# Kernel tuning notes

Hardware: AMD Instinct MI355X
Metric: run time of the kernel (lower is better)

The kernel has to match this reference:

```python
import jax, jax.numpy as jnp
import numpy as np

IN_F = 4096
OUT_F = 4096
N_VALS = 4096
N_TOKENS = 4096


def setup_inputs() -> dict:
    key = jax.random.key(0)
    k_x, k_v, k_i = jax.random.split(key, 3)
    x = jax.random.normal(k_x, (N_TOKENS, IN_F), dtype=jnp.float32)
    # codebook of memristor conductance differences (sorted, as in load_values)
    values = jnp.sort(jax.random.normal(k_v, (N_VALS,), dtype=jnp.float32))
    w_idx = jax.random.randint(k_i, (OUT_F, IN_F), 0, N_VALS, dtype=jnp.int64)
    bias = jnp.zeros((OUT_F,), dtype=jnp.float32)
    return {"x": x, "values": values, "w_idx": w_idx, "bias": bias}


def reference(x, values, w_idx, bias):
    # dequantize weight from codebook: (out_f, in_f)
    weight = values[w_idx]
    # F.linear(x, weight, bias) == x @ weight.T + bias
    return jnp.einsum("ti,oi->to", x, weight) + bias
```

## Files before the change

kernel.cpp:

```cpp
#include <hip/hip_runtime.h>
#include <hip/hip_bf16.h>
#include <stdint.h>

typedef unsigned short u16;
typedef __bf16 bf16x8 __attribute__((ext_vector_type(8)));
typedef float  f32x4  __attribute__((ext_vector_type(4)));
typedef u16    u16x8  __attribute__((ext_vector_type(8)));
typedef u16    u16x4  __attribute__((ext_vector_type(4)));

__device__ __forceinline__ u16 f2bf(float f) {
  union { float f; unsigned u; } v; v.f = f;
  unsigned u = v.u;
  unsigned r = u + 0x7FFFu + ((u >> 16) & 1u);
  return (u16)(r >> 16);
}

__device__ __forceinline__ void gld_lds16(const void* g, void* l) {
  __builtin_amdgcn_global_load_lds(
      (const __attribute__((address_space(1))) void*)g,
      (__attribute__((address_space(3))) void*)l, 16, 0, 0);
}

__global__ void detect_idx_width(const unsigned* __restrict__ w, int* __restrict__ flag) {
  unsigned v = w[threadIdx.x * 2 + 1];
  unsigned long long any = __ballot(v != 0u);
  if (threadIdx.x == 0) *flag = (any != 0ull) ? 1 : 0;
}

__global__ __launch_bounds__(256) void cvt_x_kernel(const float4* __restrict__ x,
                                                    u16* __restrict__ xb, long n8) {
  long i = (long)blockIdx.x * blockDim.x + threadIdx.x;
  long stride = (long)gridDim.x * blockDim.x;
  for (; i < n8; i += stride) {
    float4 a = x[2 * i];
    float4 b = x[2 * i + 1];
    u16x8 r;
    r[0] = f2bf(a.x); r[1] = f2bf(a.y); r[2] = f2bf(a.z); r[3] = f2bf(a.w);
    r[4] = f2bf(b.x); r[5] = f2bf(b.y); r[6] = f2bf(b.z); r[7] = f2bf(b.w);
    *(u16x8*)(xb + 8 * i) = r;
  }
}

__global__ __launch_bounds__(256) void dequant_w_kernel(const int4* __restrict__ widx,
                                                        const float* __restrict__ values,
                                                        u16* __restrict__ wb,
                                                        const int* __restrict__ flag, long n4) {
  const bool is32 = (*flag != 0);
  long i = (long)blockIdx.x * blockDim.x + threadIdx.x;
  long stride = (long)gridDim.x * blockDim.x;
  for (; i < n4; i += stride) {
    int i0, i1, i2, i3;
    if (is32) {
      int4 v = widx[i];
      i0 = v.x; i1 = v.y; i2 = v.z; i3 = v.w;
    } else {
      int4 a = widx[2 * i];
      int4 b = widx[2 * i + 1];
      i0 = a.x; i1 = a.z; i2 = b.x; i3 = b.z;
    }
    u16x4 r;
    r[0] = f2bf(values[i0]); r[1] = f2bf(values[i1]);
    r[2] = f2bf(values[i2]); r[3] = f2bf(values[i3]);
    *(u16x4*)(wb + 4 * i) = r;
  }
}

#define VMW(n) asm volatile("s_waitcnt vmcnt(" #n ")" ::: "memory")
#define LGKM0  asm volatile("s_waitcnt lgkmcnt(0)" ::: "memory")
#define SB0    __builtin_amdgcn_sched_barrier(0)
#define PH_BAR __builtin_amdgcn_s_barrier()

__global__ __launch_bounds__(512, 2) void gemm256_kernel(
    const u16* __restrict__ Xb, const u16* __restrict__ Wb,
    const float* __restrict__ bias, float* __restrict__ C,
    int Nout, int Kin) {
  __shared__ __align__(16) char lds[163840];

  const int tid  = threadIdx.x;
  const int lane = tid & 63;
  const int wave = tid >> 6;
  const int wr = wave >> 2;
  const int wc = wave & 3;

  const int nwg = gridDim.x;
  const int bid = blockIdx.x;
  const int q8 = nwg >> 3, r8 = nwg & 7;
  const int xcd = bid & 7;
  const int wg = (xcd < r8 ? xcd * (q8 + 1) : r8 * (q8 + 1) + (xcd - r8) * q8) + (bid >> 3);

  const int tiles_n = Nout / 256;
  const long brow = (long)(wg / tiles_n) * 256;
  const long bcol = (long)(wg % tiles_n) * 256;

  const size_t rowbytes = (size_t)Kin * 2;

  const int f0  = tid * 16;
  const int f1  = f0 + 8192;
  const int rS0 = f0 >> 7;
  const int rS1 = rS0 + 64;
  const int cS  = (f0 & 127) ^ ((rS0 & 7) << 4);

  const char* gA00 = (const char*)Xb + (size_t)(brow +       rS0) * rowbytes + cS;
  const char* gA01 = (const char*)Xb + (size_t)(brow +       rS1) * rowbytes + cS;
  const char* gA10 = (const char*)Xb + (size_t)(brow + 128 + rS0) * rowbytes + cS;
  const char* gA11 = (const char*)Xb + (size_t)(brow + 128 + rS1) * rowbytes + cS;
  const char* gB00 = (const char*)Wb + (size_t)(bcol +       rS0) * rowbytes + cS;
  const char* gB01 = (const char*)Wb + (size_t)(bcol +       rS1) * rowbytes + cS;
  const char* gB10 = (const char*)Wb + (size_t)(bcol + 128 + rS0) * rowbytes + cS;
  const char* gB11 = (const char*)Wb + (size_t)(bcol + 128 + rS1) * rowbytes + cS;

#define STAGE_AH(base_, h, t) { \
  gld_lds16(gA##h##0 + (size_t)(t) * 128, lds + (base_) + (h) * 16384 + f0); \
  gld_lds16(gA##h##1 + (size_t)(t) * 128, lds + (base_) + (h) * 16384 + f1); }
#define STAGE_BH(base_, h, t) { \
  gld_lds16(gB##h##0 + (size_t)(t) * 128, lds + (base_) + (h) * 16384 + f0); \
  gld_lds16(gB##h##1 + (size_t)(t) * 128, lds + (base_) + (h) * 16384 + f1); }

  const int fr   = lane & 15;
  const int kb   = (lane >> 4) * 16;
  const int xsw  = (fr & 7) << 4;
  const int colx0 = kb ^ xsw;
  const int colx1 = (64 + kb) ^ xsw;
  const int aOff = wr * 16384 + fr * 128;
  const int bOff = (wc >> 1) * 16384 + ((wc & 1) * 64 + fr) * 128;

  bf16x8 afr[2][2];
  bf16x8 bfrE[4][2];
  bf16x8 bfrO[4][2];
  f32x4  acc[8][4] = {};

#define READ_AQ(abase_, q) { \
  const char* ab = lds + (abase_) + aOff + (q) * 4096; \
  afr[0][0] = *(const bf16x8*)(ab + colx0); \
  afr[0][1] = *(const bf16x8*)(ab + colx1); \
  afr[1][0] = *(const bf16x8*)(ab + 2048 + colx0); \
  afr[1][1] = *(const bf16x8*)(ab + 2048 + colx1); }

#define READ_BPF(bbase_, dst, lo) { \
  const char* bb = lds + (bbase_) + bOff; \
  dst[(lo)][0]     = *(const bf16x8*)(bb + (lo) * 2048 + colx0); \
  dst[(lo)][1]     = *(const bf16x8*)(bb + (lo) * 2048 + colx1); \
  dst[(lo) + 1][0] = *(const bf16x8*)(bb + ((lo) + 1) * 2048 + colx0); \
  dst[(lo) + 1][1] = *(const bf16x8*)(bb + ((lo) + 1) * 2048 + colx1); }

#define MFMA_Q(q, B) { \
  __builtin_amdgcn_s_setprio(1); \
  _Pragma("unroll") for (int m2 = 0; m2 < 2; ++m2) \
  _Pragma("unroll") for (int ni = 0; ni < 4; ++ni) { \
    acc[(q)*2+m2][ni] = __builtin_amdgcn_mfma_f32_16x16x32_bf16(afr[m2][0], B[ni][0], acc[(q)*2+m2][ni], 0, 0, 0); \
    acc[(q)*2+m2][ni] = __builtin_amdgcn_mfma_f32_16x16x32_bf16(afr[m2][1], B[ni][1], acc[(q)*2+m2][ni], 0, 0, 0); } \
  __builtin_amdgcn_s_setprio(0); }

#define PHASE2(AB, q, B, EXTRA, WT) { \
  READ_AQ(AB, q); \
  EXTRA; \
  SB0; PH_BAR; LGKM0; SB0; \
  MFMA_Q(q, B); \
  SB0; WT; PH_BAR; }

  const int aB0 = 0, aB1 = 32768;
  int bR0 = 65536, bR1 = 98304, bR2 = 131072;
  const int NT = Kin >> 6;

  STAGE_AH(aB0, 0, 0); STAGE_AH(aB0, 1, 0);
  STAGE_BH(bR0, 0, 0); STAGE_BH(bR0, 1, 0);
  if (NT > 1) { STAGE_BH(bR1, 0, 1); STAGE_BH(bR1, 1, 1); }
  if (NT > 2) { STAGE_BH(bR2, 0, 2); STAGE_BH(bR2, 1, 2); }
  VMW(0);
  PH_BAR;
  READ_BPF(bR0, bfrE, 0); READ_BPF(bR0, bfrE, 2);

  const int NITER = NT >> 1;
  for (int i = 0; i < NITER; ++i) {
    const int t0 = i * 2;
    const bool gA2 = (t0 + 2 < NT);
    const bool gB3 = (t0 + 3 < NT);
    const bool gB4 = (t0 + 4 < NT);

    PHASE2(aB0, 0, bfrE, STAGE_AH(aB1, 0, t0 + 1), (void)0);
    PHASE2(aB0, 1, bfrE, { READ_BPF(bR1, bfrO, 0); STAGE_AH(aB1, 1, t0 + 1); }, (void)0);
    PHASE2(aB0, 2, bfrE, { READ_BPF(bR1, bfrO, 2); if (gB3) STAGE_BH(bR0, 0, t0 + 3); }, (void)0);
    PHASE2(aB0, 3, bfrE, { if (gB3) STAGE_BH(bR0, 1, t0 + 3); },
           { if (gB3) { VMW(2); } else { VMW(0); } });

    PHASE2(aB1, 0, bfrO, { if (gA2) STAGE_AH(aB0, 0, t0 + 2); }, (void)0);
    PHASE2(aB1, 1, bfrO, { if (gA2) { READ_BPF(bR2, bfrE, 0); STAGE_AH(aB0, 1, t0 + 2); } }, (void)0);
    PHASE2(aB1, 2, bfrO, { if (gA2) READ_BPF(bR2, bfrE, 2); if (gB4) STAGE_BH(bR1, 0, t0 + 4); }, (void)0);
    PHASE2(aB1, 3, bfrO, { if (gB4) STAGE_BH(bR1, 1, t0 + 4); },
           { if (gB4) { VMW(2); } else { VMW(0); } });

    int tmp = bR0; bR0 = bR2; bR2 = bR1; bR1 = tmp;
  }

  const int cm = (lane >> 4) * 4;
  const int cn = lane & 15;
  float bv[4];
#pragma unroll
  for (int ni = 0; ni < 4; ++ni) bv[ni] = bias[bcol + wc * 64 + ni * 16 + cn];

#pragma unroll
  for (int mi = 0; mi < 8; ++mi) {
    const long row0 = brow + wr * 128 + mi * 16 + cm;
#pragma unroll
    for (int ni = 0; ni < 4; ++ni) {
      const long col = bcol + wc * 64 + ni * 16 + cn;
#pragma unroll
      for (int j = 0; j < 4; ++j)
        C[(row0 + j) * (long)Nout + col] = acc[mi][ni][j] + bv[ni];
    }
  }
#undef STAGE_AH
#undef STAGE_BH
#undef READ_AQ
#undef READ_BPF
#undef MFMA_Q
#undef PHASE2
}

__global__ __launch_bounds__(256, 2) void gemm128_kernel(
    const u16* __restrict__ Xb, const u16* __restrict__ Wb,
    const float* __restrict__ bias, float* __restrict__ C,
    int Nout, int Kin) {
  __shared__ __align__(16) u16 As[128 * 32];
  __shared__ __align__(16) u16 Bs[128 * 32];
  const int tid  = threadIdx.x;
  const int lane = tid & 63;
  const int wave = tid >> 6;
  const int wr = wave >> 1, wc = wave & 1;
  const int nwg = gridDim.x, bid = blockIdx.x;
  const int q = nwg >> 3, r8 = nwg & 7;
  const int xcd = bid & 7;
  const int wg = (xcd < r8 ? xcd * (q + 1) : r8 * (q + 1) + (xcd - r8) * q) + (bid >> 3);
  const int tiles_n = Nout / 128;
  const long brow = (long)(wg / tiles_n) * 128;
  const long bcol = (long)(wg % tiles_n) * 128;
  const int f0 = tid * 16, f1 = f0 + 4096;
  const size_t rowbytes = (size_t)Kin * 2;
  const char* gA0 = (const char*)Xb + (size_t)(brow + (f0 >> 6)) * rowbytes + (f0 & 63);
  const char* gA1 = (const char*)Xb + (size_t)(brow + (f1 >> 6)) * rowbytes + (f1 & 63);
  const char* gB0 = (const char*)Wb + (size_t)(bcol + (f0 >> 6)) * rowbytes + (f0 & 63);
  const char* gB1 = (const char*)Wb + (size_t)(bcol + (f1 >> 6)) * rowbytes + (f1 & 63);
  char* lA0 = (char*)As + f0; char* lA1 = (char*)As + f1;
  char* lB0 = (char*)Bs + f0; char* lB1 = (char*)Bs + f1;
  const int fr = lane & 15, kb = (lane >> 4) * 16;
  const char* aptr[4]; const char* bptr[4];
#pragma unroll
  for (int i = 0; i < 4; ++i) {
    aptr[i] = (const char*)As + (wr * 64 + i * 16 + fr) * 64 + kb;
    bptr[i] = (const char*)Bs + (wc * 64 + i * 16 + fr) * 64 + kb;
  }
  f32x4 acc[4][4] = {};
  for (int kk = 0; kk < Kin; kk += 32) {
    const size_t ko = (size_t)kk * 2;
    gld_lds16(gA0 + ko, lA0); gld_lds16(gA1 + ko, lA1);
    gld_lds16(gB0 + ko, lB0); gld_lds16(gB1 + ko, lB1);
    __syncthreads();
    bf16x8 a[4], b[4];
#pragma unroll
    for (int i = 0; i < 4; ++i) a[i] = *(const bf16x8*)aptr[i];
#pragma unroll
    for (int i = 0; i < 4; ++i) b[i] = *(const bf16x8*)bptr[i];
#pragma unroll
    for (int mi = 0; mi < 4; ++mi)
#pragma unroll
      for (int ni = 0; ni < 4; ++ni)
        acc[mi][ni] = __builtin_amdgcn_mfma_f32_16x16x32_bf16(a[mi], b[ni], acc[mi][ni], 0, 0, 0);
    __syncthreads();
  }
  const int cm = (lane >> 4) * 4, cn = lane & 15;
  float bv[4];
#pragma unroll
  for (int ni = 0; ni < 4; ++ni) bv[ni] = bias[bcol + wc * 64 + ni * 16 + cn];
#pragma unroll
  for (int mi = 0; mi < 4; ++mi) {
    const long row0 = brow + wr * 64 + mi * 16 + cm;
#pragma unroll
    for (int ni = 0; ni < 4; ++ni) {
      const long col = bcol + wc * 64 + ni * 16 + cn;
#pragma unroll
      for (int j = 0; j < 4; ++j)
        C[(row0 + j) * (long)Nout + col] = acc[mi][ni][j] + bv[ni];
    }
  }
}

__global__ void fallback_kernel(const float* __restrict__ x, const float* __restrict__ values,
                                const int* __restrict__ widx, const float* __restrict__ bias,
                                float* __restrict__ out, const int* __restrict__ flag,
                                int NT, int IF, int OF) {
  const int o = blockIdx.x * blockDim.x + threadIdx.x;
  const int t = blockIdx.y;
  if (o >= OF || t >= NT) return;
  const bool is32 = (*flag != 0);
  const float* xr = x + (size_t)t * IF;
  float sum = 0.f;
  if (is32) {
    const int* w = widx + (size_t)o * IF;
    for (int k = 0; k < IF; ++k) sum += xr[k] * values[w[k]];
  } else {
    const long long* w = (const long long*)widx + (size_t)o * IF;
    for (int k = 0; k < IF; ++k) sum += xr[k] * values[(int)w[k]];
  }
  out[(size_t)t * OF + o] = sum + bias[o];
}

extern "C" void kernel_launch(void* const* d_in, const int* in_sizes, int n_in,
                              void* d_out, int out_size, void* d_ws, size_t ws_size,
                              hipStream_t stream) {
  const float* x      = (const float*)d_in[0];
  const float* values = (const float*)d_in[1];
  const int*   widx   = (const int*)d_in[2];
  const float* bias   = (const float*)d_in[3];
  float* out = (float*)d_out;

  const long xsz = in_sizes[0];
  const int  OF  = in_sizes[3];
  const long wsz = in_sizes[2];
  const int  IF  = (int)(wsz / OF);
  const int  NTOK = (int)(xsz / IF);

  u16* xb = (u16*)d_ws;
  u16* wb = xb + (size_t)NTOK * IF;
  int* flag = (int*)(wb + (size_t)OF * IF);
  const size_t need = ((size_t)NTOK * IF + (size_t)OF * IF) * sizeof(u16) + 64;

  const bool pre_ok = (ws_size >= need) && ((xsz % 8) == 0) && ((wsz % 4) == 0);
  const bool f256 = pre_ok && (IF % 128 == 0) && (IF >= 256) &&
                    (NTOK % 256 == 0) && (OF % 256 == 0);
  const bool f128 = pre_ok && (IF % 32 == 0) && (NTOK % 128 == 0) && (OF % 128 == 0);

  if (f256 || f128) {
    hipLaunchKernelGGL(detect_idx_width, dim3(1), dim3(64), 0, stream,
                       (const unsigned*)widx, flag);
    hipLaunchKernelGGL(cvt_x_kernel, dim3(2048), dim3(256), 0, stream,
                       (const float4*)x, xb, xsz / 8);
    hipLaunchKernelGGL(dequant_w_kernel, dim3(2048), dim3(256), 0, stream,
                       (const int4*)widx, values, wb, (const int*)flag, wsz / 4);
    if (f256) {
      const int grid = (NTOK / 256) * (OF / 256);
      hipLaunchKernelGGL(gemm256_kernel, dim3(grid), dim3(512), 0, stream,
                         xb, wb, bias, out, OF, IF);
    } else {
      const int grid = (NTOK / 128) * (OF / 128);
      hipLaunchKernelGGL(gemm128_kernel, dim3(grid), dim3(256), 0, stream,
                         xb, wb, bias, out, OF, IF);
    }
  } else {
    int* flag2 = (int*)d_ws;
    hipLaunchKernelGGL(detect_idx_width, dim3(1), dim3(64), 0, stream,
                       (const unsigned*)widx, flag2);
    hipLaunchKernelGGL(fallback_kernel, dim3((OF + 255) / 256, NTOK), dim3(256), 0, stream,
                       x, values, widx, bias, out, (const int*)flag2, NTOK, IF, OF);
  }
}
```

Baseline: 170.5 us.

## Double-buffer A fragments to overlap LDS reads with MFMA in GEMM loop

```diff
diff --git a/kernel.cpp b/kernel.cpp
--- a/kernel.cpp
+++ b/kernel.cpp
@@ -66,7 +66,6 @@
 }
 
 #define VMW(n) asm volatile("s_waitcnt vmcnt(" #n ")" ::: "memory")
-#define LGKM0  asm volatile("s_waitcnt lgkmcnt(0)" ::: "memory")
 #define SB0    __builtin_amdgcn_sched_barrier(0)
 #define PH_BAR __builtin_amdgcn_s_barrier()
 
@@ -124,17 +123,18 @@
   const int aOff = wr * 16384 + fr * 128;
   const int bOff = (wc >> 1) * 16384 + ((wc & 1) * 64 + fr) * 128;
 
-  bf16x8 afr[2][2];
+  bf16x8 afr0[2][2];
+  bf16x8 afr1[2][2];
   bf16x8 bfrE[4][2];
   bf16x8 bfrO[4][2];
   f32x4  acc[8][4] = {};
 
-#define READ_AQ(abase_, q) { \
+#define READ_AQ(abase_, q, DST) { \
   const char* ab = lds + (abase_) + aOff + (q) * 4096; \
-  afr[0][0] = *(const bf16x8*)(ab + colx0); \
-  afr[0][1] = *(const bf16x8*)(ab + colx1); \
-  afr[1][0] = *(const bf16x8*)(ab + 2048 + colx0); \
-  afr[1][1] = *(const bf16x8*)(ab + 2048 + colx1); }
+  DST[0][0] = *(const bf16x8*)(ab + colx0); \
+  DST[0][1] = *(const bf16x8*)(ab + colx1); \
+  DST[1][0] = *(const bf16x8*)(ab + 2048 + colx0); \
+  DST[1][1] = *(const bf16x8*)(ab + 2048 + colx1); }
 
 #define READ_BPF(bbase_, dst, lo) { \
   const char* bb = lds + (bbase_) + bOff; \
@@ -143,20 +143,16 @@
   dst[(lo) + 1][0] = *(const bf16x8*)(bb + ((lo) + 1) * 2048 + colx0); \
   dst[(lo) + 1][1] = *(const bf16x8*)(bb + ((lo) + 1) * 2048 + colx1); }
 
-#define MFMA_Q(q, B) { \
+#define MFMA_Q(q, AF, BF) { \
   __builtin_amdgcn_s_setprio(1); \
   _Pragma("unroll") for (int m2 = 0; m2 < 2; ++m2) \
   _Pragma("unroll") for (int ni = 0; ni < 4; ++ni) { \
-    acc[(q)*2+m2][ni] = __builtin_amdgcn_mfma_f32_16x16x32_bf16(afr[m2][0], B[ni][0], acc[(q)*2+m2][ni], 0, 0, 0); \
-    acc[(q)*2+m2][ni] = __builtin_amdgcn_mfma_f32_16x16x32_bf16(afr[m2][1], B[ni][1], acc[(q)*2+m2][ni], 0, 0, 0); } \
+    acc[(q)*2+m2][ni] = __builtin_amdgcn_mfma_f32_16x16x32_bf16(AF[m2][0], BF[ni][0], acc[(q)*2+m2][ni], 0, 0, 0); \
+    acc[(q)*2+m2][ni] = __builtin_amdgcn_mfma_f32_16x16x32_bf16(AF[m2][1], BF[ni][1], acc[(q)*2+m2][ni], 0, 0, 0); } \
   __builtin_amdgcn_s_setprio(0); }
 
-#define PHASE2(AB, q, B, EXTRA, WT) { \
-  READ_AQ(AB, q); \
-  EXTRA; \
-  SB0; PH_BAR; LGKM0; SB0; \
-  MFMA_Q(q, B); \
-  SB0; WT; PH_BAR; }
+#define PHASE(RDS, STG, MF, WT) { \
+  RDS; STG; SB0; PH_BAR; SB0; MF; SB0; WT; PH_BAR; }
 
   const int aB0 = 0, aB1 = 32768;
   int bR0 = 65536, bR1 = 98304, bR2 = 131072;
@@ -169,25 +165,43 @@
   VMW(0);
   PH_BAR;
   READ_BPF(bR0, bfrE, 0); READ_BPF(bR0, bfrE, 2);
+  READ_AQ(aB0, 0, afr0);
 
   const int NITER = NT >> 1;
   for (int i = 0; i < NITER; ++i) {
     const int t0 = i * 2;
-    const bool gA2 = (t0 + 2 < NT);
-    const bool gB3 = (t0 + 3 < NT);
-    const bool gB4 = (t0 + 4 < NT);
-
-    PHASE2(aB0, 0, bfrE, STAGE_AH(aB1, 0, t0 + 1), (void)0);
-    PHASE2(aB0, 1, bfrE, { READ_BPF(bR1, bfrO, 0); STAGE_AH(aB1, 1, t0 + 1); }, (void)0);
-    PHASE2(aB0, 2, bfrE, { READ_BPF(bR1, bfrO, 2); if (gB3) STAGE_BH(bR0, 0, t0 + 3); }, (void)0);
-    PHASE2(aB0, 3, bfrE, { if (gB3) STAGE_BH(bR0, 1, t0 + 3); },
-           { if (gB3) { VMW(2); } else { VMW(0); } });
-
-    PHASE2(aB1, 0, bfrO, { if (gA2) STAGE_AH(aB0, 0, t0 + 2); }, (void)0);
-    PHASE2(aB1, 1, bfrO, { if (gA2) { READ_BPF(bR2, bfrE, 0); STAGE_AH(aB0, 1, t0 + 2); } }, (void)0);
-    PHASE2(aB1, 2, bfrO, { if (gA2) READ_BPF(bR2, bfrE, 2); if (gB4) STAGE_BH(bR1, 0, t0 + 4); }, (void)0);
-    PHASE2(aB1, 3, bfrO, { if (gB4) STAGE_BH(bR1, 1, t0 + 4); },
-           { if (gB4) { VMW(2); } else { VMW(0); } });
+    const bool a1 = (t0 + 1 < NT);
+    const bool a2 = (t0 + 2 < NT);
+    const bool b3 = (t0 + 3 < NT);
+    const bool b4 = (t0 + 4 < NT);
+
+    PHASE(READ_AQ(aB0, 1, afr1),
+          { if (a1) STAGE_AH(aB1, 0, t0 + 1); },
+          MFMA_Q(0, afr0, bfrE), (void)0);
+    PHASE({ READ_AQ(aB0, 2, afr0); READ_BPF(bR1, bfrO, 0); },
+          { if (a1) STAGE_AH(aB1, 1, t0 + 1); },
+          MFMA_Q(1, afr1, bfrE), (void)0);
+    PHASE({ READ_AQ(aB0, 3, afr1); READ_BPF(bR1, bfrO, 2); },
+          { if (b3) STAGE_BH(bR0, 0, t0 + 3); },
+          MFMA_Q(2, afr0, bfrE),
+          { if (b3) { VMW(2); } else { VMW(0); } });
+    PHASE({ if (a1) READ_AQ(aB1, 0, afr0); },
+          { if (b3) STAGE_BH(bR0, 1, t0 + 3); },
+          MFMA_Q(3, afr1, bfrE), (void)0);
+
+    PHASE(READ_AQ(aB1, 1, afr1),
+          { if (a2) STAGE_AH(aB0, 0, t0 + 2); },
+          MFMA_Q(0, afr0, bfrO), (void)0);
+    PHASE({ READ_AQ(aB1, 2, afr0); if (a2) READ_BPF(bR2, bfrE, 0); },
+          { if (a2) STAGE_AH(aB0, 1, t0 + 2); },
+          MFMA_Q(1, afr1, bfrO), (void)0);
+    PHASE({ READ_AQ(aB1, 3, afr1); if (a2) READ_BPF(bR2, bfrE, 2); },
+          { if (b4) STAGE_BH(bR1, 0, t0 + 4); },
+          MFMA_Q(2, afr0, bfrO),
+          { if (b4) { VMW(2); } else { VMW(0); } });
+    PHASE({ if (a2) READ_AQ(aB0, 0, afr0); },
+          { if (b4) STAGE_BH(bR1, 1, t0 + 4); },
+          MFMA_Q(3, afr1, bfrO), (void)0);
 
     int tmp = bR0; bR0 = bR2; bR2 = bR1; bR1 = tmp;
   }
@@ -214,7 +228,7 @@
 #undef READ_AQ
 #undef READ_BPF
 #undef MFMA_Q
-#undef PHASE2
+#undef PHASE
 }
 
 __global__ __launch_bounds__(256, 2) void gemm128_kernel(
```

After: 248.4 us. 1.46x slower.
